# Kernel tuning notes

Measured on AMD Instinct MI355X. Metric: run time of the kernel, lower is better.

The kernel has to match this reference:

```python
import jax, jax.numpy as jnp
import numpy as np

B, D, K = 32768, 256, 1024


def setup_inputs() -> dict:
    key = jax.random.key(0)
    k1, k2 = jax.random.split(key)
    embedding = jax.random.normal(k1, (B, D), dtype=jnp.float32)
    codebook = jax.random.normal(k2, (K, D), dtype=jnp.float32)
    return {"embedding": embedding, "codebook": codebook}


def reference(embedding, codebook):
    # code_norms: (K,) squared L2 norm of each code
    code_norms = jnp.sum(codebook ** 2, axis=1)            # (K,)
    dots = embedding @ codebook.T                           # (B, K)
    alpha = dots / code_norms[None, :]                      # (B, K)
    # error for projecting e onto line of code c:
    #   ||e - alpha c||^2 = ||e||^2 - dots^2 / ||c||^2
    # (identical math to materializing (B,K,D) diff, without the blowup)
    e_norms = jnp.sum(embedding ** 2, axis=1, keepdims=True)  # (B, 1)
    errors = e_norms - dots ** 2 / code_norms[None, :]        # (B, K)
    indices = jnp.argmin(errors, axis=1)                      # (B,)
    # gather chosen projection: alpha[b, idx[b]] * codebook[idx[b]]
    alpha_sel = jnp.take_along_axis(alpha, indices[:, None], axis=1)  # (B, 1)
    z_out = alpha_sel * codebook[indices]                     # (B, D)
    return (z_out, indices)
```

## Files before the change

kernel.cpp:

```cpp
#include <hip/hip_runtime.h>
#include <cstdint>

#define B_ROWS 32768
#define DIM    256
#define KCODES 1024
#define NSPLIT 2

typedef _Float16 f16x8 __attribute__((ext_vector_type(8)));
typedef float    f32x4 __attribute__((ext_vector_type(4)));


__global__ __launch_bounds__(64) void vq_prep(const float* __restrict__ cb,
                                              _Float16* __restrict__ hi,
                                              _Float16* __restrict__ lo,
                                              float* __restrict__ ivs) {
  const int k = blockIdx.x;
  const int lane = threadIdx.x;
  float4 c = reinterpret_cast<const float4*>(cb)[k * 64 + lane];
  float nrm = c.x * c.x + c.y * c.y + c.z * c.z + c.w * c.w;
#pragma unroll
  for (int off = 32; off; off >>= 1) nrm += __shfl_xor(nrm, off);
  const float invn = 1.0f / sqrtf(nrm);
  if (lane == 0) ivs[k] = invn;

  float f[4] = {c.x * invn, c.y * invn, c.z * invn, c.w * invn};
  _Float16 h[4], l[4];
#pragma unroll
  for (int i = 0; i < 4; ++i) {
    h[i] = (_Float16)f[i];
    l[i] = (_Float16)((f[i] - (float)h[i]) * 2048.0f);
  }
  const int phys = (lane >> 1) ^ (k & 15);
  const int byteoff = k * 512 + phys * 16 + (lane & 1) * 8;
  *reinterpret_cast<uint2*>((char*)hi + byteoff) = *reinterpret_cast<uint2*>(h);
  *reinterpret_cast<uint2*>((char*)lo + byteoff) = *reinterpret_cast<uint2*>(l);
}

__device__ __forceinline__ void gld16(const void* g, void* l) {
  __builtin_amdgcn_global_load_lds(
      (const __attribute__((address_space(1))) uint32_t*)g,
      (__attribute__((address_space(3))) uint32_t*)l, 16, 0, 0);
}

__global__ __launch_bounds__(256, 1) void vq_main(const float* __restrict__ emb,
                                                  const _Float16* __restrict__ cbh,
                                                  const _Float16* __restrict__ cbl,
                                                  float2* __restrict__ cand) {
  __shared__ uint4 Btile[2][2048];

  const int flat = threadIdx.x;
  const int wave = flat >> 6;
  const int lane = flat & 63;
  const int quad = lane >> 4;
  const int lr   = lane & 15;

  const int split  = blockIdx.x & (NSPLIT - 1);
  const int rowblk = blockIdx.x >> 1;
  const int code0  = split * 512;

  f16x8 Ah[4][8], Al[4][8];
  const int row0 = rowblk * 256 + wave * 64;
#pragma unroll
  for (int s = 0; s < 4; ++s) {
    const float* rp = emb + (size_t)(row0 + s * 16 + lr) * DIM;
#pragma unroll
    for (int c = 0; c < 8; ++c) {
      const float* p = rp + c * 32 + quad * 8;
      float4 f0 = *reinterpret_cast<const float4*>(p);
      float4 f1 = *reinterpret_cast<const float4*>(p + 4);
      float f[8] = {f0.x, f0.y, f0.z, f0.w, f1.x, f1.y, f1.z, f1.w};
      f16x8 h, l;
#pragma unroll
      for (int j = 0; j < 8; ++j) {
        _Float16 hv = (_Float16)f[j];
        h[j] = hv;
        l[j] = (_Float16)((f[j] - (float)hv) * 2048.0f);
      }
      Ah[s][c] = h;
      Al[s][c] = l;
    }
  }

  auto stage = [&](int buf, int ch) {
    const int cbase = code0 + ch * 32;
    char* dst = (char*)&Btile[buf][0];
    const int off = wave * 2048 + lane * 16;
#pragma unroll
    for (int r = 0; r < 4; ++r) {
      const char* src = (const char*)((r & 1) ? cbl : cbh) + (cbase + (r >> 1) * 16) * 512;
      gld16(src + off,        dst + r * 8192 + off);
      gld16(src + off + 1024, dst + r * 8192 + off + 1024);
    }
  };
  stage(0, 0);

  float bg[16], bd[16];
  int   bk[16];
#pragma unroll
  for (int i = 0; i < 16; ++i) { bg[i] = -1.0f; bd[i] = 0.0f; bk[i] = code0; }

  __syncthreads();
  for (int ch = 0; ch < 16; ++ch) {
    const char* base = (const char*)&Btile[ch & 1][0];
    if (ch + 1 < 16) stage((ch + 1) & 1, ch + 1);

#pragma unroll
    for (int tt = 0; tt < 2; ++tt) {
      f32x4 aA[4], aB[4], aC[4];
#pragma unroll
      for (int s = 0; s < 4; ++s) {
        aA[s] = (f32x4){0, 0, 0, 0};
        aB[s] = (f32x4){0, 0, 0, 0};
        aC[s] = (f32x4){0, 0, 0, 0};
      }
#pragma unroll
      for (int c = 0; c < 8; ++c) {
        const int g = (((c * 4 + quad) ^ lr) * 16) + lr * 512;
        f16x8 bh = *reinterpret_cast<const f16x8*>(base + tt * 16384 + g);
        f16x8 bl = *reinterpret_cast<const f16x8*>(base + tt * 16384 + 8192 + g);
#pragma unroll
        for (int s = 0; s < 4; ++s)
          aA[s] = __builtin_amdgcn_mfma_f32_16x16x32_f16(Ah[s][c], bh, aA[s], 0, 0, 0);
#pragma unroll
        for (int s = 0; s < 4; ++s)
          aB[s] = __builtin_amdgcn_mfma_f32_16x16x32_f16(Al[s][c], bh, aB[s], 0, 0, 0);
#pragma unroll
        for (int s = 0; s < 4; ++s)
          aC[s] = __builtin_amdgcn_mfma_f32_16x16x32_f16(Ah[s][c], bl, aC[s], 0, 0, 0);
      }

      const int n = code0 + ch * 32 + tt * 16 + lr;
#pragma unroll
      for (int s = 0; s < 4; ++s)
#pragma unroll
        for (int r = 0; r < 4; ++r) {
          float x = aB[s][r] + aC[s][r];
          float d = fmaf(x, 4.8828125e-4f, aA[s][r]);
          float g = d * d;
          const int i = (s << 2) | r;
          if (g > bg[i]) { bg[i] = g; bd[i] = d; bk[i] = n; }
        }
    }
    if (ch + 1 < 16) __syncthreads();
  }

#pragma unroll
  for (int s = 0; s < 4; ++s) {
#pragma unroll
    for (int r = 0; r < 4; ++r) {
      const int i = (s << 2) | r;
      float g = bg[i]; int k = bk[i]; float d = bd[i];
#pragma unroll
      for (int m = 1; m < 16; m <<= 1) {
        float g2 = __shfl_xor(g, m);
        int   k2 = __shfl_xor(k, m);
        float d2 = __shfl_xor(d, m);
        if (g2 > g || (g2 == g && k2 < k)) { g = g2; k = k2; d = d2; }
      }
      if (lr == 0) {
        const int row = row0 + s * 16 + quad * 4 + r;
        cand[(size_t)split * B_ROWS + row] = make_float2(d, __int_as_float(k));
      }
    }
  }
}

__global__ __launch_bounds__(256) void vq_reduce(const float2* __restrict__ cand,
                                                 const float* __restrict__ ivs,
                                                 const float* __restrict__ cb,
                                                 float* __restrict__ out) {
  const int wave = threadIdx.x >> 6;
  const int lane = threadIdx.x & 63;
  const int row = blockIdx.x * 4 + wave;

  float best_g = -1.0f, best_d = 0.0f;
  int best_k = 0;
#pragma unroll
  for (int s = 0; s < NSPLIT; ++s) {
    float2 c = cand[(size_t)s * B_ROWS + row];
    int k = __float_as_int(c.y);
    float g = c.x * c.x;
    if (g > best_g || (g == best_g && k < best_k)) {
      best_g = g; best_d = c.x; best_k = k;
    }
  }
  const float alpha = best_d * ivs[best_k];
  float4 c4 = reinterpret_cast<const float4*>(cb)[best_k * 64 + lane];
  float4 z = {alpha * c4.x, alpha * c4.y, alpha * c4.z, alpha * c4.w};
  reinterpret_cast<float4*>(out)[(size_t)row * 64 + lane] = z;
  if (lane == 0) out[(size_t)B_ROWS * DIM + row] = (float)best_k;
}

extern "C" void kernel_launch(void* const* d_in, const int* in_sizes, int n_in,
                              void* d_out, int out_size, void* d_ws, size_t ws_size,
                              hipStream_t stream) {
  const float* emb = (const float*)d_in[0];
  const float* cb  = (const float*)d_in[1];
  _Float16* cbh = (_Float16*)d_ws;
  _Float16* cbl = (_Float16*)((char*)d_ws + (512 << 10));
  float*    ivs = (float*)((char*)d_ws + (1 << 20));
  float2*   cand = (float2*)((char*)d_ws + (1 << 20) + 4096);

  vq_prep<<<KCODES, 64, 0, stream>>>(cb, cbh, cbl, ivs);
  vq_main<<<(B_ROWS / 256) * NSPLIT, 256, 0, stream>>>(emb, cbh, cbl, cand);
  vq_reduce<<<B_ROWS / 4, 256, 0, stream>>>(cand, ivs, cb, (float*)d_out);
}
```

Measured before the change: 157.9 us.

## Switch VQ main kernel to 32x32x16 MFMA with smaller blocks and interleaved codebook layout

Replaces the 16x16x32 MFMA tiling (4 subtiles per wave over 64 rows) with a single 32x32x16 MFMA accumulator per wave over 32 rows. Blocks shrink to 128 threads with two blocks per CU allowed. The prep kernel now writes hi and lo codebook halves into a chunk-interleaved layout so each stage is one contiguous 16 KB copy. The per-lane best tracking drops the stored squared value and recomputes it from the kept dot. Each codebook tile is now shared by fewer rows, so LDS traffic per MFMA rises, in exchange for higher occupancy and larger MFMA instructions.

```diff
diff --git a/kernel.cpp b/kernel.cpp
--- a/kernel.cpp
+++ b/kernel.cpp
@@ -6,13 +6,12 @@
 #define KCODES 1024
 #define NSPLIT 2
 
-typedef _Float16 f16x8 __attribute__((ext_vector_type(8)));
-typedef float    f32x4 __attribute__((ext_vector_type(4)));
+typedef _Float16 f16x8  __attribute__((ext_vector_type(8)));
+typedef float    f32x16 __attribute__((ext_vector_type(16)));
 
 
 __global__ __launch_bounds__(64) void vq_prep(const float* __restrict__ cb,
-                                              _Float16* __restrict__ hi,
-                                              _Float16* __restrict__ lo,
+                                              char* __restrict__ cbq,
                                               float* __restrict__ ivs) {
   const int k = blockIdx.x;
   const int lane = threadIdx.x;
@@ -30,10 +29,14 @@
     h[i] = (_Float16)f[i];
     l[i] = (_Float16)((f[i] - (float)h[i]) * 2048.0f);
   }
-  const int phys = (lane >> 1) ^ (k & 15);
-  const int byteoff = k * 512 + phys * 16 + (lane & 1) * 8;
-  *reinterpret_cast<uint2*>((char*)hi + byteoff) = *reinterpret_cast<uint2*>(h);
-  *reinterpret_cast<uint2*>((char*)lo + byteoff) = *reinterpret_cast<uint2*>(l);
+  const int g = lane >> 1;
+  const int jd = g >> 4;
+  const int gl = g & 15;
+  const int phys = gl ^ (k & 15);
+  char* base = cbq + (size_t)(k >> 5) * 32768 + jd * 16384 +
+               (k & 31) * 256 + phys * 16 + (lane & 1) * 8;
+  *reinterpret_cast<uint2*>(base)        = *reinterpret_cast<uint2*>(h);
+  *reinterpret_cast<uint2*>(base + 8192) = *reinterpret_cast<uint2*>(l);
 }
 
 __device__ __forceinline__ void gld16(const void* g, void* l) {
@@ -42,125 +45,101 @@
       (__attribute__((address_space(3))) uint32_t*)l, 16, 0, 0);
 }
 
-__global__ __launch_bounds__(256, 1) void vq_main(const float* __restrict__ emb,
-                                                  const _Float16* __restrict__ cbh,
-                                                  const _Float16* __restrict__ cbl,
+__global__ __launch_bounds__(128, 2) void vq_main(const float* __restrict__ emb,
+                                                  const char* __restrict__ cbq,
                                                   float2* __restrict__ cand) {
-  __shared__ uint4 Btile[2][2048];
+  __shared__ uint4 Btile[2][1024];
 
   const int flat = threadIdx.x;
   const int wave = flat >> 6;
   const int lane = flat & 63;
-  const int quad = lane >> 4;
-  const int lr   = lane & 15;
+  const int n    = lane & 31;
+  const int hh   = lane >> 5;
 
   const int split  = blockIdx.x & (NSPLIT - 1);
   const int rowblk = blockIdx.x >> 1;
   const int code0  = split * 512;
+  const int row0   = rowblk * 64 + wave * 32;
 
-  f16x8 Ah[4][8], Al[4][8];
-  const int row0 = rowblk * 256 + wave * 64;
+  f16x8 Ah[16], Al[16];
+  {
+    const float* rp = emb + (size_t)(row0 + n) * DIM;
 #pragma unroll
-  for (int s = 0; s < 4; ++s) {
-    const float* rp = emb + (size_t)(row0 + s * 16 + lr) * DIM;
-#pragma unroll
-    for (int c = 0; c < 8; ++c) {
-      const float* p = rp + c * 32 + quad * 8;
+    for (int c = 0; c < 16; ++c) {
+      const float* p = rp + c * 16 + hh * 8;
       float4 f0 = *reinterpret_cast<const float4*>(p);
       float4 f1 = *reinterpret_cast<const float4*>(p + 4);
       float f[8] = {f0.x, f0.y, f0.z, f0.w, f1.x, f1.y, f1.z, f1.w};
-      f16x8 h, l;
+      f16x8 hv, lv;
 #pragma unroll
       for (int j = 0; j < 8; ++j) {
-        _Float16 hv = (_Float16)f[j];
-        h[j] = hv;
-        l[j] = (_Float16)((f[j] - (float)hv) * 2048.0f);
+        _Float16 t = (_Float16)f[j];
+        hv[j] = t;
+        lv[j] = (_Float16)((f[j] - (float)t) * 2048.0f);
       }
-      Ah[s][c] = h;
-      Al[s][c] = l;
+      Ah[c] = hv;
+      Al[c] = lv;
     }
   }
 
-  auto stage = [&](int buf, int ch) {
-    const int cbase = code0 + ch * 32;
+  auto stage = [&](int buf, int idx) {
+    const char* src = cbq + (size_t)(code0 / 32 + (idx >> 1)) * 32768 + (idx & 1) * 16384;
     char* dst = (char*)&Btile[buf][0];
-    const int off = wave * 2048 + lane * 16;
+    const int off = flat * 16;
 #pragma unroll
-    for (int r = 0; r < 4; ++r) {
-      const char* src = (const char*)((r & 1) ? cbl : cbh) + (cbase + (r >> 1) * 16) * 512;
-      gld16(src + off,        dst + r * 8192 + off);
-      gld16(src + off + 1024, dst + r * 8192 + off + 1024);
-    }
+    for (int r = 0; r < 8; ++r)
+      gld16(src + r * 2048 + off, dst + r * 2048 + off);
   };
   stage(0, 0);
 
-  float bg[16], bd[16];
+  float bd[16];
   int   bk[16];
 #pragma unroll
-  for (int i = 0; i < 16; ++i) { bg[i] = -1.0f; bd[i] = 0.0f; bk[i] = code0; }
+  for (int i = 0; i < 16; ++i) { bd[i] = 0.0f; bk[i] = code0; }
 
   __syncthreads();
-  for (int ch = 0; ch < 16; ++ch) {
-    const char* base = (const char*)&Btile[ch & 1][0];
-    if (ch + 1 < 16) stage((ch + 1) & 1, ch + 1);
-
+  for (int t = 0; t < 16; ++t) {
+    f32x16 aA = {}, aB = {}, aC = {};
 #pragma unroll
-    for (int tt = 0; tt < 2; ++tt) {
-      f32x4 aA[4], aB[4], aC[4];
-#pragma unroll
-      for (int s = 0; s < 4; ++s) {
-        aA[s] = (f32x4){0, 0, 0, 0};
-        aB[s] = (f32x4){0, 0, 0, 0};
-        aC[s] = (f32x4){0, 0, 0, 0};
-      }
+    for (int j = 0; j < 2; ++j) {
+      const int idx = t * 2 + j;
+      if (idx + 1 < 32) stage((idx + 1) & 1, idx + 1);
+      const char* base = (const char*)&Btile[idx & 1][0];
 #pragma unroll
       for (int c = 0; c < 8; ++c) {
-        const int g = (((c * 4 + quad) ^ lr) * 16) + lr * 512;
-        f16x8 bh = *reinterpret_cast<const f16x8*>(base + tt * 16384 + g);
-        f16x8 bl = *reinterpret_cast<const f16x8*>(base + tt * 16384 + 8192 + g);
+        const int xg = ((c * 2 + hh) ^ n) & 15;
+        const int a  = n * 256 + xg * 16;
+        f16x8 bh = *reinterpret_cast<const f16x8*>(base + a);
+        f16x8 bl = *reinterpret_cast<const f16x8*>(base + 8192 + a);
+        const int cg = j * 8 + c;
+        aA = __builtin_amdgcn_mfma_f32_32x32x16_f16(Ah[cg], bh, aA, 0, 0, 0);
+        aB = __builtin_amdgcn_mfma_f32_32x32x16_f16(Al[cg], bh, aB, 0, 0, 0);
+        aC = __builtin_amdgcn_mfma_f32_32x32x16_f16(Ah[cg], bl, aC, 0, 0, 0);
+      }
+      if (idx + 1 < 32) __syncthreads();
+    }
+    const int nc = code0 + t * 32 + n;
 #pragma unroll
-        for (int s = 0; s < 4; ++s)
-          aA[s] = __builtin_amdgcn_mfma_f32_16x16x32_f16(Ah[s][c], bh, aA[s], 0, 0, 0);
-#pragma unroll
-        for (int s = 0; s < 4; ++s)
-          aB[s] = __builtin_amdgcn_mfma_f32_16x16x32_f16(Al[s][c], bh, aB[s], 0, 0, 0);
-#pragma unroll
-        for (int s = 0; s < 4; ++s)
-          aC[s] = __builtin_amdgcn_mfma_f32_16x16x32_f16(Ah[s][c], bl, aC[s], 0, 0, 0);
-      }
-
-      const int n = code0 + ch * 32 + tt * 16 + lr;
-#pragma unroll
-      for (int s = 0; s < 4; ++s)
-#pragma unroll
-        for (int r = 0; r < 4; ++r) {
-          float x = aB[s][r] + aC[s][r];
-          float d = fmaf(x, 4.8828125e-4f, aA[s][r]);
-          float g = d * d;
-          const int i = (s << 2) | r;
-          if (g > bg[i]) { bg[i] = g; bd[i] = d; bk[i] = n; }
-        }
+    for (int r = 0; r < 16; ++r) {
+      float d = fmaf(aB[r] + aC[r], 4.8828125e-4f, aA[r]);
+      float g = d * d;
+      if (g > bd[r] * bd[r]) { bd[r] = d; bk[r] = nc; }
     }
-    if (ch + 1 < 16) __syncthreads();
   }
 
 #pragma unroll
-  for (int s = 0; s < 4; ++s) {
+  for (int r = 0; r < 16; ++r) {
+    float d = bd[r]; int k = bk[r];
 #pragma unroll
-    for (int r = 0; r < 4; ++r) {
-      const int i = (s << 2) | r;
-      float g = bg[i]; int k = bk[i]; float d = bd[i];
-#pragma unroll
-      for (int m = 1; m < 16; m <<= 1) {
-        float g2 = __shfl_xor(g, m);
-        int   k2 = __shfl_xor(k, m);
-        float d2 = __shfl_xor(d, m);
-        if (g2 > g || (g2 == g && k2 < k)) { g = g2; k = k2; d = d2; }
-      }
-      if (lr == 0) {
-        const int row = row0 + s * 16 + quad * 4 + r;
-        cand[(size_t)split * B_ROWS + row] = make_float2(d, __int_as_float(k));
-      }
+    for (int m = 1; m < 32; m <<= 1) {
+      float d2 = __shfl_xor(d, m);
+      int   k2 = __shfl_xor(k, m);
+      float g = d * d, g2 = d2 * d2;
+      if (g2 > g || (g2 == g && k2 < k)) { d = d2; k = k2; }
+    }
+    if (n == 0) {
+      const int row = row0 + (r & 3) + 8 * (r >> 2) + 4 * hh;
+      cand[(size_t)split * B_ROWS + row] = make_float2(d, __int_as_float(k));
     }
   }
 }
@@ -173,16 +152,14 @@
   const int lane = threadIdx.x & 63;
   const int row = blockIdx.x * 4 + wave;
 
-  float best_g = -1.0f, best_d = 0.0f;
-  int best_k = 0;
+  float best_d = 0.0f;
+  int best_k = KCODES;
 #pragma unroll
   for (int s = 0; s < NSPLIT; ++s) {
     float2 c = cand[(size_t)s * B_ROWS + row];
     int k = __float_as_int(c.y);
-    float g = c.x * c.x;
-    if (g > best_g || (g == best_g && k < best_k)) {
-      best_g = g; best_d = c.x; best_k = k;
-    }
+    float g = c.x * c.x, gb = best_d * best_d;
+    if (g > gb || (g == gb && k < best_k)) { best_d = c.x; best_k = k; }
   }
   const float alpha = best_d * ivs[best_k];
   float4 c4 = reinterpret_cast<const float4*>(cb)[best_k * 64 + lane];
@@ -196,12 +173,11 @@
                               hipStream_t stream) {
   const float* emb = (const float*)d_in[0];
   const float* cb  = (const float*)d_in[1];
-  _Float16* cbh = (_Float16*)d_ws;
-  _Float16* cbl = (_Float16*)((char*)d_ws + (512 << 10));
-  float*    ivs = (float*)((char*)d_ws + (1 << 20));
-  float2*   cand = (float2*)((char*)d_ws + (1 << 20) + 4096);
+  char*   cbq  = (char*)d_ws;
+  float*  ivs  = (float*)((char*)d_ws + (1 << 20));
+  float2* cand = (float2*)((char*)d_ws + (1 << 20) + 4096);
 
-  vq_prep<<<KCODES, 64, 0, stream>>>(cb, cbh, cbl, ivs);
-  vq_main<<<(B_ROWS / 256) * NSPLIT, 256, 0, stream>>>(emb, cbh, cbl, cand);
+  vq_prep<<<KCODES, 64, 0, stream>>>(cb, cbq, ivs);
+  vq_main<<<(B_ROWS / 64) * NSPLIT, 128, 0, stream>>>(emb, cbq, cand);
   vq_reduce<<<B_ROWS / 4, 256, 0, stream>>>(cand, ivs, cb, (float*)d_out);
 }
```

After: 153.7 us. 1.03x faster.
